# Kernel optimization log

Hardware: AMD Instinct MI355X
Metric: run time of the kernel (lower is better)

## Reference

```python
import jax, jax.numpy as jnp
import numpy as np

B = 16384  # batch
D = 64     # input_size (number of causal nodes)
H = 64     # hidden_size of each per-node MLP


def setup_inputs() -> dict:
    key = jax.random.key(0)
    k1, k2, k3 = jax.random.split(key, 3)
    inputs = jax.random.normal(k1, (B, D), dtype=jnp.float32)
    adjacency = jnp.ones((D, D), dtype=jnp.float32)  # buffer initialized to ones
    # stacked per-node weights: net_i = Linear(D->H, no bias) -> ReLU -> Linear(H->1, no bias)
    W1 = jax.random.normal(k2, (D, H, D), dtype=jnp.float32) * (1.0 / np.sqrt(D))
    W2 = jax.random.normal(k3, (D, H), dtype=jnp.float32) * (1.0 / np.sqrt(H))
    return {"inputs": inputs, "adjacency": adjacency, "W1": W1, "W2": W2}


def reference(inputs, adjacency, W1, W2):
    # inputs: [B, D]; adjacency: [D, D]; W1: [D, H, D]; W2: [D, H]
    # Original: repeat inputs to [B, D, D], mask rows by adjacency, then for each
    # node i apply its tiny MLP to row i and concat the scalar outputs -> [B, D].
    masked = inputs[:, None, :] * adjacency[None, :, :]          # [B, D, D]
    h = jax.nn.relu(jnp.einsum('bid,ihd->bih', masked, W1))      # [B, D, H]
    out = jnp.einsum('bih,ih->bi', h, W2)                        # [B, D]
    return out
```

## Files before the change

### kernel.cpp

```cpp
#include <hip/hip_runtime.h>
#include <hip/hip_bf16.h>

constexpr int BN = 16384;
constexpr int DN = 64;
constexpr int HN = 64;
constexpr int XELEMS  = BN * DN;
constexpr int W1ELEMS = DN * HN * DN;
constexpr int XCH = XELEMS / 4;
constexpr int WCH = W1ELEMS / 4;

typedef __attribute__((ext_vector_type(8))) short short8;
typedef __attribute__((ext_vector_type(4))) float f32x4;

__device__ __forceinline__ unsigned short f2bf(float f) {
    __hip_bfloat16 h = __float2bfloat16(f);
    return *reinterpret_cast<unsigned short*>(&h);
}

#define DPP_ROR_ADD(x, N)                                                     \
    x += __int_as_float(__builtin_amdgcn_update_dpp(                          \
            0, __float_as_int(x), 0x120 + (N), 0xf, 0xf, false))

__global__ __launch_bounds__(256) void prep_kernel(
    const float* __restrict__ X, const float* __restrict__ adj,
    const float* __restrict__ W1,
    unsigned short* __restrict__ Xbf, unsigned short* __restrict__ W1bf)
{
    int t = blockIdx.x * 256 + threadIdx.x;
    if (t < XCH) {
        float4 v = reinterpret_cast<const float4*>(X)[t];
        ushort4 o;
        o.x = f2bf(v.x); o.y = f2bf(v.y); o.z = f2bf(v.z); o.w = f2bf(v.w);
        reinterpret_cast<ushort4*>(Xbf)[t] = o;
    } else {
        int c = t - XCH;
        if (c < WCH) {
            int flat = c * 4;
            int i = flat >> 12;
            int d = flat & 63;
            float4 w = reinterpret_cast<const float4*>(W1)[c];
            float4 a = *reinterpret_cast<const float4*>(adj + i * DN + d);
            ushort4 o;
            o.x = f2bf(w.x * a.x); o.y = f2bf(w.y * a.y);
            o.z = f2bf(w.z * a.z); o.w = f2bf(w.w * a.w);
            reinterpret_cast<ushort4*>(W1bf)[c] = o;
        }
    }
}

__global__ __launch_bounds__(256, 4) void mlp_kernel(
    const unsigned short* __restrict__ Xbf,
    const unsigned short* __restrict__ W1bf,
    const float* __restrict__ W2,
    float* __restrict__ out)
{
    const int ng    = blockIdx.x & 15;
    const int btile = blockIdx.x >> 4;
    const int wave  = threadIdx.x >> 6;
    const int lane  = threadIdx.x & 63;
    const int row16 = lane & 15;
    const int quad  = lane >> 4;

    __shared__ unsigned short ldsW1[4 * HN * DN];
    __shared__ float ldsW2[4 * HN];
    __shared__ float lds_out[128][4];

    const int b0 = btile * 128 + wave * 32;
    const unsigned short* aBase = Xbf + (size_t)(b0 + row16) * DN + quad * 8;
    short8 afrag[2][2];
#pragma unroll
    for (int mt = 0; mt < 2; ++mt)
#pragma unroll
        for (int kk = 0; kk < 2; ++kk)
            afrag[mt][kk] = *reinterpret_cast<const short8*>(aBase + mt * 16 * DN + kk * 32);

    {
        const unsigned short* gsrc = W1bf + (size_t)ng * (4 * HN * DN);
#pragma unroll
        for (int it = 0; it < 8; ++it) {
            int chunk = it * 256 + threadIdx.x;
            int nl = chunk >> 9;
            int rem = chunk & 511;
            int h = rem >> 3;
            int c = rem & 7;
            short8 v = *reinterpret_cast<const short8*>(gsrc + chunk * 8);
            int elem = nl * 4096 + h * 64 + ((c ^ (h & 7)) << 3);
            *reinterpret_cast<short8*>(&ldsW1[elem]) = v;
        }
        if (threadIdx.x < 256)
            ldsW2[threadIdx.x] = W2[ng * 256 + threadIdx.x];
    }
    __syncthreads();

    for (int j = 0; j < 4; ++j) {
        short8 bfrag[2][4];
#pragma unroll
        for (int kk = 0; kk < 2; ++kk)
#pragma unroll
            for (int nt = 0; nt < 4; ++nt) {
                int h = nt * 16 + row16;
                int elem = j * 4096 + h * 64 + (((kk * 4 + quad) ^ (row16 & 7)) << 3);
                bfrag[kk][nt] = *reinterpret_cast<const short8*>(&ldsW1[elem]);
            }

        float w2v[4];
#pragma unroll
        for (int nt = 0; nt < 4; ++nt)
            w2v[nt] = ldsW2[j * 64 + nt * 16 + row16];

        f32x4 acc[2][4];
#pragma unroll
        for (int mt = 0; mt < 2; ++mt)
#pragma unroll
            for (int nt = 0; nt < 4; ++nt)
                acc[mt][nt] = (f32x4){0.f, 0.f, 0.f, 0.f};

#pragma unroll
        for (int kk = 0; kk < 2; ++kk)
#pragma unroll
            for (int nt = 0; nt < 4; ++nt) {
                acc[0][nt] = __builtin_amdgcn_mfma_f32_16x16x32_bf16(afrag[0][kk], bfrag[kk][nt], acc[0][nt], 0, 0, 0);
                acc[1][nt] = __builtin_amdgcn_mfma_f32_16x16x32_bf16(afrag[1][kk], bfrag[kk][nt], acc[1][nt], 0, 0, 0);
            }

#pragma unroll
        for (int mt = 0; mt < 2; ++mt) {
            float p[4];
#pragma unroll
            for (int r = 0; r < 4; ++r) {
                float q0 = fmaxf(acc[mt][0][r], 0.f) * w2v[0];
                float q1 = fmaxf(acc[mt][1][r], 0.f) * w2v[1];
                q0 = fmaf(fmaxf(acc[mt][2][r], 0.f), w2v[2], q0);
                q1 = fmaf(fmaxf(acc[mt][3][r], 0.f), w2v[3], q1);
                p[r] = q0 + q1;
                DPP_ROR_ADD(p[r], 8);
                DPP_ROR_ADD(p[r], 4);
                DPP_ROR_ADD(p[r], 2);
                DPP_ROR_ADD(p[r], 1);
            }
            if (row16 < 4)
                lds_out[wave * 32 + mt * 16 + quad * 4 + row16][j] = p[row16];
        }
    }

    __syncthreads();
    if (threadIdx.x < 128) {
        int row = threadIdx.x;
        float4 v = *reinterpret_cast<const float4*>(&lds_out[row][0]);
        *reinterpret_cast<float4*>(out + (size_t)(btile * 128 + row) * DN + ng * 4) = v;
    }
}

extern "C" void kernel_launch(void* const* d_in, const int* in_sizes, int n_in,
                              void* d_out, int out_size, void* d_ws, size_t ws_size,
                              hipStream_t stream) {
    const float* X   = (const float*)d_in[0];
    const float* adj = (const float*)d_in[1];
    const float* W1  = (const float*)d_in[2];
    const float* W2  = (const float*)d_in[3];
    float* out = (float*)d_out;

    unsigned short* Xbf  = (unsigned short*)d_ws;
    unsigned short* W1bf = Xbf + XELEMS;

    prep_kernel<<<(XCH + WCH + 255) / 256, 256, 0, stream>>>(X, adj, W1, Xbf, W1bf);
    mlp_kernel<<<(BN / 128) * 16, 256, 0, stream>>>(Xbf, W1bf, W2, out);
}
```

Measured before the change: 81.53 us.

## Fuse X bf16 conversion into MLP kernel and reorder block mapping

Drops the separate fp32-to-bf16 conversion of X from the prep kernel. The MLP kernel now loads fp32 X directly and converts it in registers, so the 2 MB bf16 X round-trip through global memory goes away. The block index mapping is swapped so consecutive blocks share the same node group, which should improve reuse of W1 in L2. It also lowers the launch-bounds occupancy hint to 3, unrolls the j loop, and uses packed f32x2 math in the epilogue. The cost is that each X tile is now read as fp32 and converted 16 times, once per node group.

```diff
diff --git a/kernel.cpp b/kernel.cpp
--- a/kernel.cpp
+++ b/kernel.cpp
@@ -4,58 +4,55 @@
 constexpr int BN = 16384;
 constexpr int DN = 64;
 constexpr int HN = 64;
-constexpr int XELEMS  = BN * DN;
 constexpr int W1ELEMS = DN * HN * DN;
-constexpr int XCH = XELEMS / 4;
 constexpr int WCH = W1ELEMS / 4;
 
 typedef __attribute__((ext_vector_type(8))) short short8;
 typedef __attribute__((ext_vector_type(4))) float f32x4;
+typedef __attribute__((ext_vector_type(2))) float f32x2;
 
 __device__ __forceinline__ unsigned short f2bf(float f) {
     __hip_bfloat16 h = __float2bfloat16(f);
     return *reinterpret_cast<unsigned short*>(&h);
 }
 
+__device__ __forceinline__ short8 cvt8(float4 a, float4 b) {
+    short8 r;
+    r[0] = (short)f2bf(a.x); r[1] = (short)f2bf(a.y);
+    r[2] = (short)f2bf(a.z); r[3] = (short)f2bf(a.w);
+    r[4] = (short)f2bf(b.x); r[5] = (short)f2bf(b.y);
+    r[6] = (short)f2bf(b.z); r[7] = (short)f2bf(b.w);
+    return r;
+}
+
 #define DPP_ROR_ADD(x, N)                                                     \
     x += __int_as_float(__builtin_amdgcn_update_dpp(                          \
             0, __float_as_int(x), 0x120 + (N), 0xf, 0xf, false))
 
-__global__ __launch_bounds__(256) void prep_kernel(
-    const float* __restrict__ X, const float* __restrict__ adj,
-    const float* __restrict__ W1,
-    unsigned short* __restrict__ Xbf, unsigned short* __restrict__ W1bf)
+__global__ __launch_bounds__(256) void w1prep_kernel(
+    const float* __restrict__ W1, const float* __restrict__ adj,
+    unsigned short* __restrict__ W1bf)
 {
-    int t = blockIdx.x * 256 + threadIdx.x;
-    if (t < XCH) {
-        float4 v = reinterpret_cast<const float4*>(X)[t];
-        ushort4 o;
-        o.x = f2bf(v.x); o.y = f2bf(v.y); o.z = f2bf(v.z); o.w = f2bf(v.w);
-        reinterpret_cast<ushort4*>(Xbf)[t] = o;
-    } else {
-        int c = t - XCH;
-        if (c < WCH) {
-            int flat = c * 4;
-            int i = flat >> 12;
-            int d = flat & 63;
-            float4 w = reinterpret_cast<const float4*>(W1)[c];
-            float4 a = *reinterpret_cast<const float4*>(adj + i * DN + d);
-            ushort4 o;
-            o.x = f2bf(w.x * a.x); o.y = f2bf(w.y * a.y);
-            o.z = f2bf(w.z * a.z); o.w = f2bf(w.w * a.w);
-            reinterpret_cast<ushort4*>(W1bf)[c] = o;
-        }
-    }
+    int c = blockIdx.x * 256 + threadIdx.x;
+    int flat = c * 4;
+    int i = flat >> 12;
+    int d = flat & 63;
+    float4 w = reinterpret_cast<const float4*>(W1)[c];
+    float4 a = *reinterpret_cast<const float4*>(adj + i * DN + d);
+    ushort4 o;
+    o.x = f2bf(w.x * a.x); o.y = f2bf(w.y * a.y);
+    o.z = f2bf(w.z * a.z); o.w = f2bf(w.w * a.w);
+    reinterpret_cast<ushort4*>(W1bf)[c] = o;
 }
 
-__global__ __launch_bounds__(256, 4) void mlp_kernel(
-    const unsigned short* __restrict__ Xbf,
+__global__ __launch_bounds__(256, 3) void mlp_kernel(
+    const float* __restrict__ X,
     const unsigned short* __restrict__ W1bf,
     const float* __restrict__ W2,
     float* __restrict__ out)
 {
-    const int ng    = blockIdx.x & 15;
-    const int btile = blockIdx.x >> 4;
+    const int btile = blockIdx.x & 127;
+    const int ng    = blockIdx.x >> 7;
     const int wave  = threadIdx.x >> 6;
     const int lane  = threadIdx.x & 63;
     const int row16 = lane & 15;
@@ -66,13 +63,17 @@
     __shared__ float lds_out[128][4];
 
     const int b0 = btile * 128 + wave * 32;
-    const unsigned short* aBase = Xbf + (size_t)(b0 + row16) * DN + quad * 8;
+    const float* aBase = X + (size_t)(b0 + row16) * DN + quad * 8;
     short8 afrag[2][2];
 #pragma unroll
     for (int mt = 0; mt < 2; ++mt)
 #pragma unroll
-        for (int kk = 0; kk < 2; ++kk)
-            afrag[mt][kk] = *reinterpret_cast<const short8*>(aBase + mt * 16 * DN + kk * 32);
+        for (int kk = 0; kk < 2; ++kk) {
+            const float* p = aBase + mt * 16 * DN + kk * 32;
+            float4 v0 = *reinterpret_cast<const float4*>(p);
+            float4 v1 = *reinterpret_cast<const float4*>(p + 4);
+            afrag[mt][kk] = cvt8(v0, v1);
+        }
 
     {
         const unsigned short* gsrc = W1bf + (size_t)ng * (4 * HN * DN);
@@ -87,11 +88,11 @@
             int elem = nl * 4096 + h * 64 + ((c ^ (h & 7)) << 3);
             *reinterpret_cast<short8*>(&ldsW1[elem]) = v;
         }
-        if (threadIdx.x < 256)
-            ldsW2[threadIdx.x] = W2[ng * 256 + threadIdx.x];
+        ldsW2[threadIdx.x] = W2[ng * 256 + threadIdx.x];
     }
     __syncthreads();
 
+#pragma unroll
     for (int j = 0; j < 4; ++j) {
         short8 bfrag[2][4];
 #pragma unroll
@@ -125,14 +126,17 @@
 
 #pragma unroll
         for (int mt = 0; mt < 2; ++mt) {
-            float p[4];
+            f32x2 s01 = (f32x2){0.f, 0.f}, s23 = (f32x2){0.f, 0.f};
+#pragma unroll
+            for (int nt = 0; nt < 4; ++nt) {
+                f32x2 m01 = (f32x2){fmaxf(acc[mt][nt][0], 0.f), fmaxf(acc[mt][nt][1], 0.f)};
+                f32x2 m23 = (f32x2){fmaxf(acc[mt][nt][2], 0.f), fmaxf(acc[mt][nt][3], 0.f)};
+                s01 += m01 * w2v[nt];
+                s23 += m23 * w2v[nt];
+            }
+            float p[4] = {s01[0], s01[1], s23[0], s23[1]};
 #pragma unroll
             for (int r = 0; r < 4; ++r) {
-                float q0 = fmaxf(acc[mt][0][r], 0.f) * w2v[0];
-                float q1 = fmaxf(acc[mt][1][r], 0.f) * w2v[1];
-                q0 = fmaf(fmaxf(acc[mt][2][r], 0.f), w2v[2], q0);
-                q1 = fmaf(fmaxf(acc[mt][3][r], 0.f), w2v[3], q1);
-                p[r] = q0 + q1;
                 DPP_ROR_ADD(p[r], 8);
                 DPP_ROR_ADD(p[r], 4);
                 DPP_ROR_ADD(p[r], 2);
@@ -160,9 +164,8 @@
     const float* W2  = (const float*)d_in[3];
     float* out = (float*)d_out;
 
-    unsigned short* Xbf  = (unsigned short*)d_ws;
-    unsigned short* W1bf = Xbf + XELEMS;
+    unsigned short* W1bf = (unsigned short*)d_ws;
 
-    prep_kernel<<<(XCH + WCH + 255) / 256, 256, 0, stream>>>(X, adj, W1, Xbf, W1bf);
-    mlp_kernel<<<(BN / 128) * 16, 256, 0, stream>>>(Xbf, W1bf, W2, out);
+    w1prep_kernel<<<WCH / 256, 256, 0, stream>>>(W1, adj, W1bf);
+    mlp_kernel<<<128 * 16, 256, 0, stream>>>(X, W1bf, W2, out);
 }
```

Result: faster. 78.85 us, median of 2 (-3.3%).
